# Kernel optimization log

Hardware: AMD Instinct MI355X
Metric: run time of the kernel (lower is better)

Reference implementation:

```python
import jax, jax.numpy as jnp
import numpy as np

# ---- config (mirrors init_kwargs) ----
D_MODEL = 1024
D_STATE = 128
EXPAND = 2
HEADDIM = 64
D_INNER = D_MODEL * EXPAND            # 2048
NHEADS = D_INNER // HEADDIM           # 32
ROPE_FRACTION = 0.5
ROTATE_DIM = (int(D_STATE * ROPE_FRACTION) // 2) * 2   # 64
NUM_ANGLES = ROTATE_DIM // 2          # 32
A_FLOOR = 1e-4
EPS = 1e-5
IN_PROJ_DIM = 2 * D_INNER + 2 * D_STATE + 3 * NHEADS + NUM_ANGLES  # 4480
BATCH, SEQLEN = 2, 2048


def _state_rmsnorm(x, w):
    rms = jnp.sqrt(jnp.mean(x * x, axis=-1, keepdims=True) + EPS)
    return x / rms * w


def _apply_rotary_pairs(x, phase):
    # x: (b,s,h,d_state), phase: (b,s,h,num_pairs)
    if ROTATE_DIM == 0:
        return x
    x_rot = x[..., :ROTATE_DIM].reshape(*x.shape[:-1], ROTATE_DIM // 2, 2)
    x_pass = x[..., ROTATE_DIM:]
    cos = jnp.cos(phase)
    sin = jnp.sin(phase)
    real = x_rot[..., 0]
    imag = x_rot[..., 1]
    rr = real * cos - imag * sin
    ri = real * sin + imag * cos
    rotated = jnp.stack([rr, ri], axis=-1).reshape(*x.shape[:-1], ROTATE_DIM)
    if x_pass.shape[-1] == 0:
        return rotated
    return jnp.concatenate([rotated, x_pass], axis=-1)


def setup_inputs() -> dict:
    key = jax.random.key(0)
    ks = jax.random.split(key, 5)
    x = jax.random.normal(ks[0], (BATCH, SEQLEN, D_MODEL), jnp.float32)
    W_in = jax.random.normal(ks[1], (IN_PROJ_DIM, D_MODEL), jnp.float32) / np.sqrt(D_MODEL)
    # dt_bias ~ inverse-softplus of dt sampled in [dt_min, dt_max]
    dt = jnp.exp(jax.random.uniform(ks[2], (NHEADS,), jnp.float32) * (np.log(0.1) - np.log(0.001)) + np.log(0.001))
    dt = jnp.clip(dt, 1e-4)
    dt_bias = dt + jnp.log(-jnp.expm1(-dt))
    B_norm_w = jnp.ones((D_STATE,), jnp.float32)
    C_norm_w = jnp.ones((D_STATE,), jnp.float32)
    B_bias = jnp.ones((NHEADS, D_STATE), jnp.float32)
    C_bias = jnp.ones((NHEADS, D_STATE), jnp.float32)
    D_param = jnp.ones((NHEADS,), jnp.float32)
    out_norm_w = jnp.ones((D_INNER,), jnp.float32)
    W_out = jax.random.normal(ks[3], (D_MODEL, D_INNER), jnp.float32) / np.sqrt(D_INNER)
    return {"x": x, "W_in": W_in, "dt_bias": dt_bias, "B_norm_w": B_norm_w,
            "C_norm_w": C_norm_w, "B_bias": B_bias, "C_bias": C_bias,
            "D_param": D_param, "out_norm_w": out_norm_w, "W_out": W_out}


def reference(x, W_in, dt_bias, B_norm_w, C_norm_w, B_bias, C_bias, D_param, out_norm_w, W_out):
    b, s, _ = x.shape
    proj = jnp.einsum('bsd,pd->bsp', x, W_in)
    sizes = [D_INNER, D_INNER, D_STATE, D_STATE, NHEADS, NHEADS, NHEADS, NUM_ANGLES]
    offs = np.cumsum([0] + sizes)
    z, v, B_raw, C_raw, dd_dt, dd_A, trap_logits, angle_logits = [
        proj[..., offs[i]:offs[i + 1]] for i in range(8)]
    z = z.reshape(b, s, NHEADS, HEADDIM)
    v = v.reshape(b, s, NHEADS, HEADDIM)
    Bm = _state_rmsnorm(B_raw, B_norm_w)[:, :, None, :] + B_bias[None, None]   # (b,s,h,n)
    Cm = _state_rmsnorm(C_raw, C_norm_w)[:, :, None, :] + C_bias[None, None]
    dt = jax.nn.softplus(dd_dt + dt_bias[None, None])          # (b,s,h)
    A = jnp.minimum(-jax.nn.softplus(dd_A), -A_FLOOR)          # (b,s,h)
    trap = jax.nn.sigmoid(trap_logits)                          # (b,s,h)
    phase = jnp.cumsum(angle_logits, axis=1)[:, :, None, :]     # (b,s,1,angles)
    phase = jnp.broadcast_to(phase, (b, s, NHEADS, NUM_ANGLES))
    Bm = _apply_rotary_pairs(Bm, phase)
    Cm = _apply_rotary_pairs(Cm, phase)

    alpha = jnp.exp(A * dt)               # (b,s,h)
    beta = (1.0 - trap) * dt * alpha
    gamma = trap * dt

    # move time to leading for scan: (s, b, h, ...)
    def tl(a):
        return jnp.moveaxis(a, 1, 0)
    xs = (tl(alpha), tl(beta), tl(gamma), tl(Bm), tl(Cm), tl(v))

    state0 = jnp.zeros((b, NHEADS, HEADDIM, D_STATE), jnp.float32)
    pk0 = jnp.zeros((b, NHEADS, D_STATE), jnp.float32)
    pv0 = jnp.zeros((b, NHEADS, HEADDIM), jnp.float32)

    def step(carry, inp):
        state, pk, pv = carry
        a_t, b_t, g_t, k_t, q_t, v_t = inp
        prev_outer = pv[..., :, None] * pk[..., None, :]        # (b,h,p,n)
        curr_outer = v_t[..., :, None] * k_t[..., None, :]
        state = (a_t[..., None, None] * state
                 + b_t[..., None, None] * prev_outer
                 + g_t[..., None, None] * curr_outer)
        y_t = jnp.einsum('bhpn,bhn->bhp', state, q_t) + D_param[None, :, None] * v_t
        return (state, k_t, v_t), y_t

    _, ys = jax.lax.scan(step, (state0, pk0, pv0), xs)
    y = jnp.moveaxis(ys, 0, 1).reshape(b, s, D_INNER)
    z = z.reshape(b, s, D_INNER)
    # GatedRMSNorm
    rms = jnp.sqrt(jnp.mean(y * y, axis=-1, keepdims=True) + EPS)
    y = (y / rms * out_norm_w) * jax.nn.silu(z)
    return jnp.einsum('bsi,di->bsd', y, W_out)
```

## Files before the change

### kernel.cpp

```cpp
#include <hip/hip_runtime.h>
#include <math.h>

#define S_LEN 2048
#define NBATCH 2
#define DMODEL 1024
#define PDIM 4480
#define DI 2048
#define NH 32
#define HD 64
#define DS 128
#define NA 32
#define CHK 64
#define NC (S_LEN / CHK)
#define OFF_Z 0
#define OFF_V 2048
#define OFF_B 4096
#define OFF_C 4224
#define OFF_DT 4352
#define OFF_A 4384
#define OFF_TRAP 4416
#define OFF_ANG 4448

typedef __attribute__((ext_vector_type(8))) short s8v;
typedef __attribute__((ext_vector_type(4))) float f4v;

__device__ __forceinline__ float softplus_f(float x) {
    return x > 20.f ? x : log1pf(expf(x));
}

__device__ __forceinline__ ushort f2bf(float f) {
    unsigned u = __float_as_uint(f);
    unsigned r = (u + 0x7fffu + ((u >> 16) & 1u)) >> 16;
    return (ushort)r;
}

__device__ __forceinline__ uint4 pack8(const float* f) {
    uint4 o;
    o.x = (unsigned)f2bf(f[0]) | ((unsigned)f2bf(f[1]) << 16);
    o.y = (unsigned)f2bf(f[2]) | ((unsigned)f2bf(f[3]) << 16);
    o.z = (unsigned)f2bf(f[4]) | ((unsigned)f2bf(f[5]) << 16);
    o.w = (unsigned)f2bf(f[6]) | ((unsigned)f2bf(f[7]) << 16);
    return o;
}

__device__ __forceinline__ float bf2f(ushort u) {
    unsigned v = ((unsigned)u) << 16;
    return __uint_as_float(v);
}

__global__ __launch_bounds__(256)
void f2bf_swz(const float* __restrict__ in, ushort* __restrict__ out,
              int nchunks, int shift) {
    int idx = blockIdx.x * 256 + threadIdx.x;
    if (idx >= nchunks) return;
    int dst = idx ^ ((idx >> shift) & 7);
    const float* ip = in + (size_t)idx * 8;
    float4 v0 = *(const float4*)ip;
    float4 v1 = *(const float4*)(ip + 4);
    uint4 o;
    o.x = (unsigned)f2bf(v0.x) | ((unsigned)f2bf(v0.y) << 16);
    o.y = (unsigned)f2bf(v0.z) | ((unsigned)f2bf(v0.w) << 16);
    o.z = (unsigned)f2bf(v1.x) | ((unsigned)f2bf(v1.y) << 16);
    o.w = (unsigned)f2bf(v1.z) | ((unsigned)f2bf(v1.w) << 16);
    *(uint4*)(out + (size_t)dst * 8) = o;
}

__global__ __launch_bounds__(256, 2)
void gemm_bf16(const ushort* __restrict__ A, const ushort* __restrict__ B,
               float* __restrict__ C, int M, int N, int K) {
    __shared__ __align__(16) short lA[128 * 64];
    __shared__ __align__(16) short lB[128 * 64];
    int nwg = gridDim.x;
    int bid = blockIdx.x;
    int q = nwg >> 3;
    int swz = (bid & 7) * q + (bid >> 3);
    int nb = N >> 7;
    int bx = swz % nb, by = swz / nb;

    int tid = threadIdx.x;
    int wv = tid >> 6, ln = tid & 63;
    int rl = ln & 15, kg = ln >> 4, r7 = rl & 7;
    int R0 = (wv >> 1) * 64, C0 = (wv & 1) * 64;

    const ushort* Ag = A + (size_t)(by * 128 + wv * 32 + (ln >> 3)) * K + (ln & 7) * 8;
    const ushort* Bg = B + (size_t)(bx * 128 + wv * 32 + (ln >> 3)) * K + (ln & 7) * 8;
    short* lAw = lA + (wv * 32) * 64;
    short* lBw = lB + (wv * 32) * 64;

    f4v acc[4][4];
#pragma unroll
    for (int m = 0; m < 4; ++m)
#pragma unroll
        for (int n = 0; n < 4; ++n) acc[m][n] = f4v{0.f, 0.f, 0.f, 0.f};

    for (int k0 = 0; k0 < K; k0 += 64) {
        __syncthreads();
#pragma unroll
        for (int i = 0; i < 4; ++i) {
            __builtin_amdgcn_global_load_lds(
                (const __attribute__((address_space(1))) void*)(Ag + (size_t)i * 8 * K + k0),
                (__attribute__((address_space(3))) void*)(lAw + i * 8 * 64), 16, 0, 0);
            __builtin_amdgcn_global_load_lds(
                (const __attribute__((address_space(1))) void*)(Bg + (size_t)i * 8 * K + k0),
                (__attribute__((address_space(3))) void*)(lBw + i * 8 * 64), 16, 0, 0);
        }
        __syncthreads();
#pragma unroll
        for (int ks = 0; ks < 2; ++ks) {
            int kc = ks * 4 + kg;
            int co = ((kc ^ r7) << 3);
            s8v av[4], bv[4];
#pragma unroll
            for (int m = 0; m < 4; ++m)
                av[m] = *(const s8v*)&lA[(R0 + m * 16 + rl) * 64 + co];
#pragma unroll
            for (int n = 0; n < 4; ++n)
                bv[n] = *(const s8v*)&lB[(C0 + n * 16 + rl) * 64 + co];
#pragma unroll
            for (int m = 0; m < 4; ++m)
#pragma unroll
                for (int n = 0; n < 4; ++n)
                    acc[m][n] = __builtin_amdgcn_mfma_f32_16x16x32_bf16(
                        av[m], bv[n], acc[m][n], 0, 0, 0);
        }
    }
#pragma unroll
    for (int m = 0; m < 4; ++m)
#pragma unroll
        for (int n = 0; n < 4; ++n) {
            size_t row0 = (size_t)(by * 128 + R0 + m * 16 + kg * 4);
            int col = bx * 128 + C0 + n * 16 + rl;
#pragma unroll
            for (int r = 0; r < 4; ++r)
                C[(row0 + r) * N + col] = acc[m][n][r];
        }
}

__global__ __launch_bounds__(256)
void phase_kernel(const float* __restrict__ proj, float* __restrict__ cosb,
                  float* __restrict__ sinb) {
    int b = blockIdx.x >> 5;
    int j = blockIdx.x & 31;
    int tid = threadIdx.x;
    __shared__ float part[256];
    float v[8];
    float run = 0.f;
#pragma unroll
    for (int e = 0; e < 8; ++e) {
        int s = tid * 8 + e;
        v[e] = proj[((size_t)(b * S_LEN + s)) * PDIM + OFF_ANG + j];
        run += v[e];
    }
    part[tid] = run;
    __syncthreads();
    for (int off = 1; off < 256; off <<= 1) {
        float add = (tid >= off) ? part[tid - off] : 0.f;
        __syncthreads();
        part[tid] += add;
        __syncthreads();
    }
    float acc = (tid > 0) ? part[tid - 1] : 0.f;
#pragma unroll
    for (int e = 0; e < 8; ++e) {
        acc += v[e];
        int s = tid * 8 + e;
        size_t o = ((size_t)(b * S_LEN + s)) * NA + j;
        cosb[o] = cosf(acc);
        sinb[o] = sinf(acc);
    }
}

__global__ __launch_bounds__(128)
void prep_kernel(const float* __restrict__ proj, const float* __restrict__ dt_bias,
                 const float* __restrict__ Bw, const float* __restrict__ Cw,
                 const float* __restrict__ cosb, const float* __restrict__ sinb,
                 float* __restrict__ Bn, float* __restrict__ Cn,
                 float* __restrict__ ldb, float* __restrict__ wbuf,
                 float* __restrict__ pubuf) {
    size_t row = blockIdx.x;
    int b = (int)(row >> 11);
    int s = (int)(row & 2047);
    int n = threadIdx.x;
    const float* pr = proj + row * PDIM;
    float vB = pr[OFF_B + n];
    float vC = pr[OFF_C + n];
    float sB = vB * vB, sC = vC * vC;
#pragma unroll
    for (int off = 32; off >= 1; off >>= 1) {
        sB += __shfl_xor(sB, off);
        sC += __shfl_xor(sC, off);
    }
    __shared__ float redB[2], redC[2];
    if ((n & 63) == 0) { redB[n >> 6] = sB; redC[n >> 6] = sC; }
    __syncthreads();
    float rB = sqrtf((redB[0] + redB[1]) * (1.f / 128.f) + 1e-5f);
    float rC = sqrtf((redC[0] + redC[1]) * (1.f / 128.f) + 1e-5f);
    float bn = vB / rB * Bw[n];
    float cn = vC / rC * Cw[n];
    float bp = __shfl_xor(bn, 1);
    float cp = __shfl_xor(cn, 1);
    float ob = bn, oc = cn;
    if (n < 64) {
        float c = cosb[row * NA + (n >> 1)];
        float sn_ = sinb[row * NA + (n >> 1)];
        if ((n & 1) == 0) { ob = bn * c - bp * sn_; oc = cn * c - cp * sn_; }
        else              { ob = bp * sn_ + bn * c; oc = cp * sn_ + cn * c; }
    }
    Bn[row * DS + n] = ob;
    Cn[row * DS + n] = oc;
    if (n < NH) {
        int h = n;
        float dtv = softplus_f(pr[OFF_DT + h] + dt_bias[h]);
        float Av = -fmaxf(softplus_f(pr[OFF_A + h]), 1e-4f);
        float trap = 1.f / (1.f + expf(-pr[OFF_TRAP + h]));
        size_t o = ((size_t)(b * NH + h)) * S_LEN + s;
        ldb[o]   = Av * dtv;
        wbuf[o]  = trap * dtv;
        pubuf[o] = (1.f - trap) * dtv;
    }
}

__global__ __launch_bounds__(256)
void lcum_kernel(float* __restrict__ ell) {
    size_t row = blockIdx.x;
    int tid = threadIdx.x;
    float* p = ell + row * S_LEN;
    float v[8];
    float run = 0.f;
#pragma unroll
    for (int e = 0; e < 8; ++e) { v[e] = p[tid * 8 + e]; run += v[e]; }
    __shared__ float part[256];
    part[tid] = run;
    __syncthreads();
    for (int off = 1; off < 256; off <<= 1) {
        float add = (tid >= off) ? part[tid - off] : 0.f;
        __syncthreads();
        part[tid] += add;
        __syncthreads();
    }
    float acc = (tid > 0) ? part[tid - 1] : 0.f;
#pragma unroll
    for (int e = 0; e < 8; ++e) { acc += v[e]; p[tid * 8 + e] = acc; }
}

__device__ __forceinline__ void build_vals32(
    float* vals, const float* __restrict__ br, const float* __restrict__ bias,
    const float* __restrict__ cr, const float* __restrict__ sr, int n0, int rot) {
    if (rot) {
#pragma unroll
        for (int a = 0; a < 16; ++a) {
            float c = cr[a], s = sr[a];
            float e = bias[n0 + 2 * a], o = bias[n0 + 2 * a + 1];
            vals[2 * a]     = br[2 * a]     + e * c - o * s;
            vals[2 * a + 1] = br[2 * a + 1] + e * s + o * c;
        }
    } else {
#pragma unroll
        for (int j = 0; j < 32; ++j) vals[j] = br[j] + bias[n0 + j];
    }
}

__global__ __launch_bounds__(256, 2)
void delta_kernel(const float* __restrict__ proj, const float* __restrict__ Bn,
                  const float* __restrict__ cosb, const float* __restrict__ sinb,
                  const float* __restrict__ ell, const float* __restrict__ wbuf,
                  const float* __restrict__ pubuf, const float* __restrict__ B_bias,
                  float* __restrict__ delta, float* __restrict__ rbuf) {
    __shared__ ushort KT[DS * CHK];
    __shared__ ushort VT[HD * CHK];
    int blk = blockIdx.x;
    int c = blk & (NC - 1);
    int h = (blk >> 5) & (NH - 1);
    int b = blk >> 10;
    int tid = threadIdx.x;
    size_t row0 = (size_t)b * S_LEN + c * CHK;
    size_t bh = (size_t)b * NH + h;
    int i = tid >> 2, q4 = tid & 3;

    size_t so = bh * S_LEN + c * CHK + i;
    float llast = ell[bh * S_LEN + c * CHK + CHK - 1];
    float u = wbuf[so];
    if (c * CHK + i < S_LEN - 1) u += pubuf[so + 1];
    float coef = expf(llast - ell[so]) * u;
    if (tid == 0) {
        float base = (c == 0) ? 0.f : ell[bh * S_LEN + c * CHK - 1];
        rbuf[blk] = expf(llast - base);
    }
    {
        int n0 = q4 * 32;
        float vals[32];
        build_vals32(vals, Bn + (row0 + i) * DS + n0, B_bias + h * DS,
                     cosb + (row0 + i) * NA + q4 * 16, sinb + (row0 + i) * NA + q4 * 16,
                     n0, q4 < 2);
#pragma unroll
        for (int j = 0; j < 32; ++j) {
            int n = n0 + j;
            KT[n * 64 + (((i >> 3) ^ (n & 7)) << 3) + (i & 7)] = f2bf(vals[j]);
        }
    }
    {
        int p0 = q4 * 16;
        const float* vr = proj + (row0 + i) * PDIM + OFF_V + h * HD + p0;
#pragma unroll
        for (int j = 0; j < 16; ++j) {
            int p = p0 + j;
            VT[p * 64 + (((i >> 3) ^ (p & 7)) << 3) + (i & 7)] = f2bf(vr[j] * coef);
        }
    }
    __syncthreads();
    int wv = tid >> 6, ln = tid & 63, rl = ln & 15, kg = ln >> 4;
    int pA = wv * 16 + rl;
    s8v aV[2];
#pragma unroll
    for (int ks = 0; ks < 2; ++ks)
        aV[ks] = *(const s8v*)&VT[pA * 64 + (((ks * 4 + kg) ^ (pA & 7)) << 3)];
    f4v dacc[8];
#pragma unroll
    for (int nt = 0; nt < 8; ++nt) dacc[nt] = f4v{0.f, 0.f, 0.f, 0.f};
#pragma unroll
    for (int nt = 0; nt < 8; ++nt) {
        int nB = nt * 16 + rl;
#pragma unroll
        for (int ks = 0; ks < 2; ++ks) {
            s8v bK = *(const s8v*)&KT[nB * 64 + (((ks * 4 + kg) ^ (nB & 7)) << 3)];
            dacc[nt] = __builtin_amdgcn_mfma_f32_16x16x32_bf16(aV[ks], bK, dacc[nt], 0, 0, 0);
        }
    }
    float* dp = delta + (bh * NC + c) * (size_t)(HD * DS);
#pragma unroll
    for (int nt = 0; nt < 8; ++nt) {
        int n = nt * 16 + rl;
#pragma unroll
        for (int r = 0; r < 4; ++r) {
            int p = wv * 16 + kg * 4 + r;
            dp[p * DS + n] = dacc[nt][r];
        }
    }
}

__global__ __launch_bounds__(256)
void state_prop(float* __restrict__ delta, const float* __restrict__ rbuf) {
    size_t bh = blockIdx.x;
    int tid = threadIdx.x;
    float4 st[8];
#pragma unroll
    for (int k = 0; k < 8; ++k) st[k] = float4{0.f, 0.f, 0.f, 0.f};
    for (int c = 0; c < NC; ++c) {
        float* dp = delta + (bh * NC + c) * (size_t)(HD * DS);
        float r = rbuf[bh * NC + c];
#pragma unroll
        for (int k = 0; k < 8; ++k) {
            int off = k * 1024 + tid * 4;
            float4 d = *(const float4*)(dp + off);
            float4 s = st[k];
            *(float4*)(dp + off) = s;
            st[k].x = fmaf(r, s.x, d.x);
            st[k].y = fmaf(r, s.y, d.y);
            st[k].z = fmaf(r, s.z, d.z);
            st[k].w = fmaf(r, s.w, d.w);
        }
    }
}

__global__ __launch_bounds__(256, 2)
void out_kernel(const float* __restrict__ proj, const float* __restrict__ Bn,
                const float* __restrict__ Cn, const float* __restrict__ cosb,
                const float* __restrict__ sinb, const float* __restrict__ ell,
                const float* __restrict__ wbuf, const float* __restrict__ pubuf,
                const float* __restrict__ B_bias, const float* __restrict__ C_bias,
                const float* __restrict__ D_param, const float* __restrict__ delta,
                float* __restrict__ y) {
    __shared__ ushort Qb[CHK * DS];
    __shared__ ushort Kb[CHK * DS];
    __shared__ ushort VTb[HD * CHK];
    __shared__ ushort PTb[CHK * CHK];
    __shared__ float s_ell[CHK], s_u[CHK], s_w[CHK], s_d[CHK];
    int blk = blockIdx.x;
    int c = blk & (NC - 1);
    int h = (blk >> 5) & (NH - 1);
    int b = blk >> 10;
    int tid = threadIdx.x;
    size_t row0 = (size_t)b * S_LEN + c * CHK;
    size_t bh = (size_t)b * NH + h;

    const float* sp0 = delta + (bh * NC + c) * (size_t)(HD * DS)
                       + (size_t)(tid >> 2) * DS + (tid & 3) * 32;
    float4 sreg[8];
#pragma unroll
    for (int j = 0; j < 8; ++j) sreg[j] = ((const float4*)sp0)[j];

    int t = tid >> 2, q4 = tid & 3;
    {
        int n0 = q4 * 32;
        float vals[32];
        build_vals32(vals, Cn + (row0 + t) * DS + n0, C_bias + h * DS,
                     cosb + (row0 + t) * NA + q4 * 16, sinb + (row0 + t) * NA + q4 * 16,
                     n0, q4 < 2);
#pragma unroll
        for (int j = 0; j < 4; ++j) {
            int cc = (q4 * 4 + j) ^ (t & 7);
            *(uint4*)&Qb[t * 128 + cc * 8] = pack8(&vals[j * 8]);
        }
    }
    {
        int n0 = q4 * 32;
        float vals[32];
        build_vals32(vals, Bn + (row0 + t) * DS + n0, B_bias + h * DS,
                     cosb + (row0 + t) * NA + q4 * 16, sinb + (row0 + t) * NA + q4 * 16,
                     n0, q4 < 2);
#pragma unroll
        for (int j = 0; j < 4; ++j) {
            int cc = (q4 * 4 + j) ^ (t & 7);
            *(uint4*)&Kb[t * 128 + cc * 8] = pack8(&vals[j * 8]);
        }
    }
    {
        int p0 = q4 * 16;
        const float* vr = proj + (row0 + t) * PDIM + OFF_V + h * HD + p0;
#pragma unroll
        for (int j = 0; j < 16; ++j) {
            int p = p0 + j;
            VTb[p * 64 + (((t >> 3) ^ (p & 7)) << 3) + (t & 7)] = f2bf(vr[j]);
        }
    }
    if (tid < CHK) {
        int tt = tid;
        size_t so = bh * S_LEN + c * CHK + tt;
        float lt = ell[so];
        s_ell[tt] = lt;
        float wv_ = wbuf[so];
        s_w[tt] = wv_;
        float u = wv_;
        if (c * CHK + tt < S_LEN - 1) u += pubuf[so + 1];
        s_u[tt] = u;
        float base = (c == 0) ? 0.f : ell[bh * S_LEN + c * CHK - 1];
        s_d[tt] = expf(lt - base);
    }
    __syncthreads();

    int wv = tid >> 6, ln = tid & 63, rl = ln & 15, kg = ln >> 4;
    int tA = wv * 16 + rl;
    s8v aQ[4];
#pragma unroll
    for (int kc = 0; kc < 4; ++kc)
        aQ[kc] = *(const s8v*)&Qb[tA * 128 + (((kc * 4 + kg) ^ (tA & 7)) << 3)];
    f4v pacc[4];
#pragma unroll
    for (int st = 0; st < 4; ++st) pacc[st] = f4v{0.f, 0.f, 0.f, 0.f};
#pragma unroll
    for (int st = 0; st < 4; ++st) {
        int sB = st * 16 + rl;
#pragma unroll
        for (int kc = 0; kc < 4; ++kc) {
            s8v bK = *(const s8v*)&Kb[sB * 128 + (((kc * 4 + kg) ^ (sB & 7)) << 3)];
            pacc[st] = __builtin_amdgcn_mfma_f32_16x16x32_bf16(aQ[kc], bK, pacc[st], 0, 0, 0);
        }
    }
#pragma unroll
    for (int st = 0; st < 4; ++st) {
        int s = st * 16 + rl;
#pragma unroll
        for (int r = 0; r < 4; ++r) {
            int t2 = wv * 16 + kg * 4 + r;
            float m;
            if (s < t2)       m = expf(s_ell[t2] - s_ell[s]) * s_u[s];
            else if (s == t2) m = s_w[t2];
            else              m = 0.f;
            PTb[t2 * 64 + (((s >> 3) ^ (t2 & 7)) << 3) + (s & 7)] = f2bf(pacc[st][r] * m);
        }
    }
    __syncthreads();
    {
        int p = tid >> 2, nq = tid & 3;
        float fv[32];
#pragma unroll
        for (int j = 0; j < 8; ++j) *(float4*)&fv[j * 4] = sreg[j];
#pragma unroll
        for (int j = 0; j < 4; ++j) {
            int cc = (nq * 4 + j) ^ (p & 7);
            *(uint4*)&Kb[p * 128 + cc * 8] = pack8(&fv[j * 8]);
        }
    }
    __syncthreads();
    s8v aP[2];
#pragma unroll
    for (int ks = 0; ks < 2; ++ks)
        aP[ks] = *(const s8v*)&PTb[tA * 64 + (((ks * 4 + kg) ^ (tA & 7)) << 3)];
    f4v y1[4], y2[4];
#pragma unroll
    for (int pt = 0; pt < 4; ++pt) { y1[pt] = f4v{0.f,0.f,0.f,0.f}; y2[pt] = f4v{0.f,0.f,0.f,0.f}; }
#pragma unroll
    for (int pt = 0; pt < 4; ++pt) {
        int pB = pt * 16 + rl;
#pragma unroll
        for (int ks = 0; ks < 2; ++ks) {
            s8v bV = *(const s8v*)&VTb[pB * 64 + (((ks * 4 + kg) ^ (pB & 7)) << 3)];
            y1[pt] = __builtin_amdgcn_mfma_f32_16x16x32_bf16(aP[ks], bV, y1[pt], 0, 0, 0);
        }
#pragma unroll
        for (int kc = 0; kc < 4; ++kc) {
            s8v bS = *(const s8v*)&Kb[pB * 128 + (((kc * 4 + kg) ^ (pB & 7)) << 3)];
            y2[pt] = __builtin_amdgcn_mfma_f32_16x16x32_bf16(aQ[kc], bS, y2[pt], 0, 0, 0);
        }
    }
    float Dp = D_param[h];
#pragma unroll
    for (int pt = 0; pt < 4; ++pt) {
#pragma unroll
        for (int r = 0; r < 4; ++r) {
            int t2 = wv * 16 + kg * 4 + r;
            int p = pt * 16 + rl;
            float v = proj[(row0 + t2) * PDIM + OFF_V + h * HD + p];
            y[(row0 + t2) * DI + h * HD + p] = y1[pt][r] + s_d[t2] * y2[pt][r] + Dp * v;
        }
    }
}

__global__ __launch_bounds__(256)
void ynorm_kernel(const float* __restrict__ y, const float* __restrict__ proj,
                  const float* __restrict__ w, ushort* __restrict__ ybf) {
    size_t row = blockIdx.x;
    int tid = threadIdx.x;
    const float* yr = y + row * (size_t)DI;
    float4 v0 = *(const float4*)(yr + tid * 8);
    float4 v1 = *(const float4*)(yr + tid * 8 + 4);
    float ss = v0.x * v0.x + v0.y * v0.y + v0.z * v0.z + v0.w * v0.w +
               v1.x * v1.x + v1.y * v1.y + v1.z * v1.z + v1.w * v1.w;
#pragma unroll
    for (int off = 32; off >= 1; off >>= 1) ss += __shfl_xor(ss, off);
    __shared__ float red[4];
    if ((tid & 63) == 0) red[tid >> 6] = ss;
    __syncthreads();
    float tot = red[0] + red[1] + red[2] + red[3];
    float rinv = 1.f / sqrtf(tot * (1.f / 2048.f) + 1e-5f);
    const float* zr = proj + row * (size_t)PDIM + OFF_Z;
    float4 z0 = *(const float4*)(zr + tid * 8);
    float4 z1 = *(const float4*)(zr + tid * 8 + 4);
    float4 w0 = *(const float4*)(w + tid * 8);
    float4 w1 = *(const float4*)(w + tid * 8 + 4);
    float yv[8] = {v0.x, v0.y, v0.z, v0.w, v1.x, v1.y, v1.z, v1.w};
    float zv[8] = {z0.x, z0.y, z0.z, z0.w, z1.x, z1.y, z1.z, z1.w};
    float wv[8] = {w0.x, w0.y, w0.z, w0.w, w1.x, w1.y, w1.z, w1.w};
    ushort u[8];
#pragma unroll
    for (int e = 0; e < 8; ++e) {
        float sil = zv[e] / (1.f + expf(-zv[e]));
        u[e] = f2bf(yv[e] * rinv * wv[e] * sil);
    }
    int dstc = (tid & ~7) | ((tid & 7) ^ ((int)row & 7));
    uint4 o;
    o.x = (unsigned)u[0] | ((unsigned)u[1] << 16);
    o.y = (unsigned)u[2] | ((unsigned)u[3] << 16);
    o.z = (unsigned)u[4] | ((unsigned)u[5] << 16);
    o.w = (unsigned)u[6] | ((unsigned)u[7] << 16);
    *(uint4*)(ybf + row * (size_t)DI + dstc * 8) = o;
}

extern "C" void kernel_launch(void* const* d_in, const int* in_sizes, int n_in,
                              void* d_out, int out_size, void* d_ws, size_t ws_size,
                              hipStream_t stream) {
    const float* x          = (const float*)d_in[0];
    const float* W_in       = (const float*)d_in[1];
    const float* dt_bias    = (const float*)d_in[2];
    const float* B_norm_w   = (const float*)d_in[3];
    const float* C_norm_w   = (const float*)d_in[4];
    const float* B_bias     = (const float*)d_in[5];
    const float* C_bias     = (const float*)d_in[6];
    const float* D_param    = (const float*)d_in[7];
    const float* out_norm_w = (const float*)d_in[8];
    const float* W_out      = (const float*)d_in[9];
    float* out = (float*)d_out;

    const size_t M = (size_t)NBATCH * S_LEN;
    float* ws = (float*)d_ws;
    size_t off = 0;
    float* proj  = ws + off; off += M * PDIM;
    float* cosb  = ws + off; off += M * NA;
    float* sinb  = ws + off; off += M * NA;
    float* Bn    = ws + off; off += M * DS;
    float* Cn    = ws + off; off += M * DS;
    float* ell   = ws + off; off += (size_t)NBATCH * NH * S_LEN;
    float* wbuf  = ws + off; off += (size_t)NBATCH * NH * S_LEN;
    float* pubuf = ws + off; off += (size_t)NBATCH * NH * S_LEN;
    float* delta = ws + off; off += (size_t)NBATCH * NH * NC * HD * DS;
    float* rbuf  = ws + off; off += (size_t)NBATCH * NH * NC;
    float* y     = ws + off; off += M * DI;
    ushort* xbf  = (ushort*)(ws + off); off += M * DMODEL / 2;
    ushort* wibf = (ushort*)(ws + off); off += (size_t)PDIM * DMODEL / 2;
    ushort* wobf = (ushort*)(ws + off); off += (size_t)DMODEL * DI / 2;
    ushort* ybf  = (ushort*)(ws + off); off += M * DI / 2;

    {
        int nc_x  = (int)(M * DMODEL / 8);
        int nc_wi = PDIM * DMODEL / 8;
        int nc_wo = DMODEL * DI / 8;
        f2bf_swz<<<dim3((nc_x + 255) / 256), 256, 0, stream>>>(x, xbf, nc_x, 7);
        f2bf_swz<<<dim3((nc_wi + 255) / 256), 256, 0, stream>>>(W_in, wibf, nc_wi, 7);
        f2bf_swz<<<dim3((nc_wo + 255) / 256), 256, 0, stream>>>(W_out, wobf, nc_wo, 8);
    }
    gemm_bf16<<<dim3((PDIM / 128) * (int)(M / 128)), 256, 0, stream>>>(xbf, wibf, proj, (int)M, PDIM, DMODEL);
    phase_kernel<<<dim3(NBATCH * NA), 256, 0, stream>>>(proj, cosb, sinb);
    prep_kernel<<<dim3((int)M), 128, 0, stream>>>(proj, dt_bias, B_norm_w, C_norm_w,
                                                  cosb, sinb, Bn, Cn, ell, wbuf, pubuf);
    lcum_kernel<<<dim3(NBATCH * NH), 256, 0, stream>>>(ell);
    delta_kernel<<<dim3(NBATCH * NH * NC), 256, 0, stream>>>(proj, Bn, cosb, sinb, ell,
                                                             wbuf, pubuf, B_bias, delta, rbuf);
    state_prop<<<dim3(NBATCH * NH), 256, 0, stream>>>(delta, rbuf);
    out_kernel<<<dim3(NBATCH * NH * NC), 256, 0, stream>>>(proj, Bn, Cn, cosb, sinb, ell,
                                                           wbuf, pubuf, B_bias, C_bias,
                                                           D_param, delta, y);
    ynorm_kernel<<<dim3((int)M), 256, 0, stream>>>(y, proj, out_norm_w, ybf);
    gemm_bf16<<<dim3((DMODEL / 128) * (int)(M / 128)), 256, 0, stream>>>(ybf, wobf, out, (int)M, DMODEL, DI);
}
```

Baseline: 267.0 us.

## Move intra-chunk work into the delta kernel and pass bf16 tiles to a lean output kernel

The delta kernel becomes bdp_kernel. It now builds Q, K and V once per chunk, computes the masked QK^T decay matrix and the chunk state delta, and writes bf16 Q, V, P and state tiles to workspace. State propagation now reads and writes bf16 states with register prefetch of the next chunk, which halves that traffic. The output kernel becomes out2_kernel, which loads the precomputed tiles straight into LDS with global_load_lds and only does the final two matmuls. This removes duplicated B/C rotation and V loading between the two chunk kernels, in exchange for extra bf16 round trips through global memory and lower state precision.

```diff
diff --git a/kernel.cpp b/kernel.cpp
--- a/kernel.cpp
+++ b/kernel.cpp
@@ -44,9 +44,10 @@
 }
 
 __device__ __forceinline__ float bf2f(ushort u) {
-    unsigned v = ((unsigned)u) << 16;
-    return __uint_as_float(v);
-}
+    return __uint_as_float(((unsigned)u) << 16);
+}
+__device__ __forceinline__ float bf_lo(unsigned u) { return __uint_as_float(u << 16); }
+__device__ __forceinline__ float bf_hi(unsigned u) { return __uint_as_float(u & 0xffff0000u); }
 
 __global__ __launch_bounds__(256)
 void f2bf_swz(const float* __restrict__ in, ushort* __restrict__ out,
@@ -260,14 +261,20 @@
     }
 }
 
-__global__ __launch_bounds__(256, 2)
-void delta_kernel(const float* __restrict__ proj, const float* __restrict__ Bn,
-                  const float* __restrict__ cosb, const float* __restrict__ sinb,
-                  const float* __restrict__ ell, const float* __restrict__ wbuf,
-                  const float* __restrict__ pubuf, const float* __restrict__ B_bias,
-                  float* __restrict__ delta, float* __restrict__ rbuf) {
-    __shared__ ushort KT[DS * CHK];
-    __shared__ ushort VT[HD * CHK];
+__global__ __launch_bounds__(256, 3)
+void bdp_kernel(const float* __restrict__ proj, const float* __restrict__ Bn,
+                const float* __restrict__ Cn, const float* __restrict__ cosb,
+                const float* __restrict__ sinb, const float* __restrict__ ell,
+                const float* __restrict__ wbuf, const float* __restrict__ pubuf,
+                const float* __restrict__ B_bias, const float* __restrict__ C_bias,
+                ushort* __restrict__ qbuf, ushort* __restrict__ vtbuf,
+                ushort* __restrict__ pbuf, ushort* __restrict__ dstate,
+                float* __restrict__ dvec, float* __restrict__ rbuf) {
+    __shared__ __align__(16) ushort Qb[CHK * DS];
+    __shared__ __align__(16) ushort Kb[CHK * DS];
+    __shared__ __align__(16) ushort cVT[HD * CHK];
+    __shared__ __align__(16) ushort PB[CHK * CHK];
+    __shared__ float s_ell[CHK], s_u[CHK], s_w[CHK];
     int blk = blockIdx.x;
     int c = blk & (NC - 1);
     int h = (blk >> 5) & (NH - 1);
@@ -279,13 +286,17 @@
 
     size_t so = bh * S_LEN + c * CHK + i;
     float llast = ell[bh * S_LEN + c * CHK + CHK - 1];
+    float li = ell[so];
     float u = wbuf[so];
     if (c * CHK + i < S_LEN - 1) u += pubuf[so + 1];
-    float coef = expf(llast - ell[so]) * u;
-    if (tid == 0) {
-        float base = (c == 0) ? 0.f : ell[bh * S_LEN + c * CHK - 1];
-        rbuf[blk] = expf(llast - base);
-    }
+    float coef = expf(llast - li) * u;
+    float base = (c == 0) ? 0.f : ell[bh * S_LEN + c * CHK - 1];
+    if (q4 == 0) {
+        s_ell[i] = li; s_u[i] = u; s_w[i] = wbuf[so];
+        dvec[(size_t)blk * CHK + i] = expf(li - base);
+    }
+    if (tid == 0) rbuf[blk] = expf(llast - base);
+
     {
         int n0 = q4 * 32;
         float vals[32];
@@ -293,9 +304,21 @@
                      cosb + (row0 + i) * NA + q4 * 16, sinb + (row0 + i) * NA + q4 * 16,
                      n0, q4 < 2);
 #pragma unroll
-        for (int j = 0; j < 32; ++j) {
-            int n = n0 + j;
-            KT[n * 64 + (((i >> 3) ^ (n & 7)) << 3) + (i & 7)] = f2bf(vals[j]);
+        for (int j = 0; j < 4; ++j) {
+            int cc = (q4 * 4 + j) ^ (i & 7);
+            *(uint4*)&Kb[i * 128 + cc * 8] = pack8(&vals[j * 8]);
+        }
+    }
+    {
+        int n0 = q4 * 32;
+        float vals[32];
+        build_vals32(vals, Cn + (row0 + i) * DS + n0, C_bias + h * DS,
+                     cosb + (row0 + i) * NA + q4 * 16, sinb + (row0 + i) * NA + q4 * 16,
+                     n0, q4 < 2);
+#pragma unroll
+        for (int j = 0; j < 4; ++j) {
+            int cc = (q4 * 4 + j) ^ (i & 7);
+            *(uint4*)&Qb[i * 128 + cc * 8] = pack8(&vals[j * 8]);
         }
     }
     {
@@ -304,156 +327,54 @@
 #pragma unroll
         for (int j = 0; j < 16; ++j) {
             int p = p0 + j;
-            VT[p * 64 + (((i >> 3) ^ (p & 7)) << 3) + (i & 7)] = f2bf(vr[j] * coef);
-        }
-    }
-    __syncthreads();
+            float v = vr[j];
+            int addr = p * 64 + (((i >> 3) ^ (p & 7)) << 3) + (i & 7);
+            PB[addr]  = f2bf(v);
+            cVT[addr] = f2bf(v * coef);
+        }
+    }
+    __syncthreads();
+
     int wv = tid >> 6, ln = tid & 63, rl = ln & 15, kg = ln >> 4;
-    int pA = wv * 16 + rl;
-    s8v aV[2];
-#pragma unroll
-    for (int ks = 0; ks < 2; ++ks)
-        aV[ks] = *(const s8v*)&VT[pA * 64 + (((ks * 4 + kg) ^ (pA & 7)) << 3)];
-    f4v dacc[8];
-#pragma unroll
-    for (int nt = 0; nt < 8; ++nt) dacc[nt] = f4v{0.f, 0.f, 0.f, 0.f};
-#pragma unroll
-    for (int nt = 0; nt < 8; ++nt) {
-        int nB = nt * 16 + rl;
-#pragma unroll
-        for (int ks = 0; ks < 2; ++ks) {
-            s8v bK = *(const s8v*)&KT[nB * 64 + (((ks * 4 + kg) ^ (nB & 7)) << 3)];
-            dacc[nt] = __builtin_amdgcn_mfma_f32_16x16x32_bf16(aV[ks], bK, dacc[nt], 0, 0, 0);
-        }
-    }
-    float* dp = delta + (bh * NC + c) * (size_t)(HD * DS);
-#pragma unroll
-    for (int nt = 0; nt < 8; ++nt) {
-        int n = nt * 16 + rl;
-#pragma unroll
-        for (int r = 0; r < 4; ++r) {
-            int p = wv * 16 + kg * 4 + r;
-            dp[p * DS + n] = dacc[nt][r];
-        }
-    }
-}
-
-__global__ __launch_bounds__(256)
-void state_prop(float* __restrict__ delta, const float* __restrict__ rbuf) {
-    size_t bh = blockIdx.x;
-    int tid = threadIdx.x;
-    float4 st[8];
-#pragma unroll
-    for (int k = 0; k < 8; ++k) st[k] = float4{0.f, 0.f, 0.f, 0.f};
-    for (int c = 0; c < NC; ++c) {
-        float* dp = delta + (bh * NC + c) * (size_t)(HD * DS);
-        float r = rbuf[bh * NC + c];
-#pragma unroll
-        for (int k = 0; k < 8; ++k) {
-            int off = k * 1024 + tid * 4;
-            float4 d = *(const float4*)(dp + off);
-            float4 s = st[k];
-            *(float4*)(dp + off) = s;
-            st[k].x = fmaf(r, s.x, d.x);
-            st[k].y = fmaf(r, s.y, d.y);
-            st[k].z = fmaf(r, s.z, d.z);
-            st[k].w = fmaf(r, s.w, d.w);
-        }
-    }
-}
-
-__global__ __launch_bounds__(256, 2)
-void out_kernel(const float* __restrict__ proj, const float* __restrict__ Bn,
-                const float* __restrict__ Cn, const float* __restrict__ cosb,
-                const float* __restrict__ sinb, const float* __restrict__ ell,
-                const float* __restrict__ wbuf, const float* __restrict__ pubuf,
-                const float* __restrict__ B_bias, const float* __restrict__ C_bias,
-                const float* __restrict__ D_param, const float* __restrict__ delta,
-                float* __restrict__ y) {
-    __shared__ ushort Qb[CHK * DS];
-    __shared__ ushort Kb[CHK * DS];
-    __shared__ ushort VTb[HD * CHK];
-    __shared__ ushort PTb[CHK * CHK];
-    __shared__ float s_ell[CHK], s_u[CHK], s_w[CHK], s_d[CHK];
-    int blk = blockIdx.x;
-    int c = blk & (NC - 1);
-    int h = (blk >> 5) & (NH - 1);
-    int b = blk >> 10;
-    int tid = threadIdx.x;
-    size_t row0 = (size_t)b * S_LEN + c * CHK;
-    size_t bh = (size_t)b * NH + h;
-
-    const float* sp0 = delta + (bh * NC + c) * (size_t)(HD * DS)
-                       + (size_t)(tid >> 2) * DS + (tid & 3) * 32;
-    float4 sreg[8];
-#pragma unroll
-    for (int j = 0; j < 8; ++j) sreg[j] = ((const float4*)sp0)[j];
-
-    int t = tid >> 2, q4 = tid & 3;
+    int tA = wv * 16 + rl;
+    s8v aQ[4];
+#pragma unroll
+    for (int kc = 0; kc < 4; ++kc)
+        aQ[kc] = *(const s8v*)&Qb[tA * 128 + (((kc * 4 + kg) ^ (tA & 7)) << 3)];
+    f4v pacc[4];
+#pragma unroll
+    for (int st = 0; st < 4; ++st) pacc[st] = f4v{0.f, 0.f, 0.f, 0.f};
+#pragma unroll
+    for (int st = 0; st < 4; ++st) {
+        int sB = st * 16 + rl;
+#pragma unroll
+        for (int kc = 0; kc < 4; ++kc) {
+            s8v bK = *(const s8v*)&Kb[sB * 128 + (((kc * 4 + kg) ^ (sB & 7)) << 3)];
+            pacc[st] = __builtin_amdgcn_mfma_f32_16x16x32_bf16(aQ[kc], bK, pacc[st], 0, 0, 0);
+        }
+    }
+    {
+        const uint4* qs = (const uint4*)Qb;
+        uint4* qd = (uint4*)(qbuf + (size_t)blk * (CHK * DS));
+#pragma unroll
+        for (int k = 0; k < 4; ++k) qd[tid + k * 256] = qs[tid + k * 256];
+        const uint4* vs = (const uint4*)PB;
+        uint4* vd = (uint4*)(vtbuf + (size_t)blk * (CHK * CHK));
+#pragma unroll
+        for (int k = 0; k < 2; ++k) vd[tid + k * 256] = vs[tid + k * 256];
+    }
+    __syncthreads();
+
     {
         int n0 = q4 * 32;
         float vals[32];
-        build_vals32(vals, Cn + (row0 + t) * DS + n0, C_bias + h * DS,
-                     cosb + (row0 + t) * NA + q4 * 16, sinb + (row0 + t) * NA + q4 * 16,
+        build_vals32(vals, Bn + (row0 + i) * DS + n0, B_bias + h * DS,
+                     cosb + (row0 + i) * NA + q4 * 16, sinb + (row0 + i) * NA + q4 * 16,
                      n0, q4 < 2);
 #pragma unroll
-        for (int j = 0; j < 4; ++j) {
-            int cc = (q4 * 4 + j) ^ (t & 7);
-            *(uint4*)&Qb[t * 128 + cc * 8] = pack8(&vals[j * 8]);
-        }
-    }
-    {
-        int n0 = q4 * 32;
-        float vals[32];
-        build_vals32(vals, Bn + (row0 + t) * DS + n0, B_bias + h * DS,
-                     cosb + (row0 + t) * NA + q4 * 16, sinb + (row0 + t) * NA + q4 * 16,
-                     n0, q4 < 2);
-#pragma unroll
-        for (int j = 0; j < 4; ++j) {
-            int cc = (q4 * 4 + j) ^ (t & 7);
-            *(uint4*)&Kb[t * 128 + cc * 8] = pack8(&vals[j * 8]);
-        }
-    }
-    {
-        int p0 = q4 * 16;
-        const float* vr = proj + (row0 + t) * PDIM + OFF_V + h * HD + p0;
-#pragma unroll
-        for (int j = 0; j < 16; ++j) {
-            int p = p0 + j;
-            VTb[p * 64 + (((t >> 3) ^ (p & 7)) << 3) + (t & 7)] = f2bf(vr[j]);
-        }
-    }
-    if (tid < CHK) {
-        int tt = tid;
-        size_t so = bh * S_LEN + c * CHK + tt;
-        float lt = ell[so];
-        s_ell[tt] = lt;
-        float wv_ = wbuf[so];
-        s_w[tt] = wv_;
-        float u = wv_;
-        if (c * CHK + tt < S_LEN - 1) u += pubuf[so + 1];
-        s_u[tt] = u;
-        float base = (c == 0) ? 0.f : ell[bh * S_LEN + c * CHK - 1];
-        s_d[tt] = expf(lt - base);
-    }
-    __syncthreads();
-
-    int wv = tid >> 6, ln = tid & 63, rl = ln & 15, kg = ln >> 4;
-    int tA = wv * 16 + rl;
-    s8v aQ[4];
-#pragma unroll
-    for (int kc = 0; kc < 4; ++kc)
-        aQ[kc] = *(const s8v*)&Qb[tA * 128 + (((kc * 4 + kg) ^ (tA & 7)) << 3)];
-    f4v pacc[4];
-#pragma unroll
-    for (int st = 0; st < 4; ++st) pacc[st] = f4v{0.f, 0.f, 0.f, 0.f};
-#pragma unroll
-    for (int st = 0; st < 4; ++st) {
-        int sB = st * 16 + rl;
-#pragma unroll
-        for (int kc = 0; kc < 4; ++kc) {
-            s8v bK = *(const s8v*)&Kb[sB * 128 + (((kc * 4 + kg) ^ (sB & 7)) << 3)];
-            pacc[st] = __builtin_amdgcn_mfma_f32_16x16x32_bf16(aQ[kc], bK, pacc[st], 0, 0, 0);
+        for (int j = 0; j < 32; ++j) {
+            int n = n0 + j;
+            Qb[n * 64 + (((i >> 3) ^ (n & 7)) << 3) + (i & 7)] = f2bf(vals[j]);
         }
     }
 #pragma unroll
@@ -466,22 +387,140 @@
             if (s < t2)       m = expf(s_ell[t2] - s_ell[s]) * s_u[s];
             else if (s == t2) m = s_w[t2];
             else              m = 0.f;
-            PTb[t2 * 64 + (((s >> 3) ^ (t2 & 7)) << 3) + (s & 7)] = f2bf(pacc[st][r] * m);
-        }
-    }
-    __syncthreads();
+            PB[t2 * 64 + (((s >> 3) ^ (t2 & 7)) << 3) + (s & 7)] = f2bf(pacc[st][r] * m);
+        }
+    }
+    __syncthreads();
+
+    int pA = wv * 16 + rl;
+    s8v aV[2];
+#pragma unroll
+    for (int ks = 0; ks < 2; ++ks)
+        aV[ks] = *(const s8v*)&cVT[pA * 64 + (((ks * 4 + kg) ^ (pA & 7)) << 3)];
+#pragma unroll
+    for (int nt = 0; nt < 8; ++nt) {
+        int nB = nt * 16 + rl;
+        f4v dacc = f4v{0.f, 0.f, 0.f, 0.f};
+#pragma unroll
+        for (int ks = 0; ks < 2; ++ks) {
+            s8v bK = *(const s8v*)&Qb[nB * 64 + (((ks * 4 + kg) ^ (nB & 7)) << 3)];
+            dacc = __builtin_amdgcn_mfma_f32_16x16x32_bf16(aV[ks], bK, dacc, 0, 0, 0);
+        }
+#pragma unroll
+        for (int r = 0; r < 4; ++r) {
+            int p = wv * 16 + kg * 4 + r;
+            int n = nt * 16 + rl;
+            Kb[p * 128 + (((n >> 3) ^ (p & 7)) << 3) + (n & 7)] = f2bf(dacc[r]);
+        }
+    }
+    __syncthreads();
+
     {
-        int p = tid >> 2, nq = tid & 3;
-        float fv[32];
-#pragma unroll
-        for (int j = 0; j < 8; ++j) *(float4*)&fv[j * 4] = sreg[j];
+        const uint4* ds_ = (const uint4*)Kb;
+        uint4* dd = (uint4*)(dstate + (size_t)blk * (CHK * DS));
+#pragma unroll
+        for (int k = 0; k < 4; ++k) dd[tid + k * 256] = ds_[tid + k * 256];
+        const uint4* ps = (const uint4*)PB;
+        uint4* pd = (uint4*)(pbuf + (size_t)blk * (CHK * CHK));
+#pragma unroll
+        for (int k = 0; k < 2; ++k) pd[tid + k * 256] = ps[tid + k * 256];
+    }
+}
+
+__global__ __launch_bounds__(256)
+void state_prop(ushort* __restrict__ dstate, const float* __restrict__ rbuf) {
+    size_t bh = blockIdx.x;
+    int tid = threadIdx.x;
+    float st[32];
+#pragma unroll
+    for (int j = 0; j < 32; ++j) st[j] = 0.f;
+    uint4* base = (uint4*)dstate;
+    size_t b0 = bh * NC * 1024ull;
+    uint4 nxt[4];
+#pragma unroll
+    for (int j = 0; j < 4; ++j) nxt[j] = base[b0 + tid * 4 + j];
+    for (int c = 0; c < NC; ++c) {
+        uint4 cur[4];
+#pragma unroll
+        for (int j = 0; j < 4; ++j) cur[j] = nxt[j];
+        if (c + 1 < NC) {
+#pragma unroll
+            for (int j = 0; j < 4; ++j)
+                nxt[j] = base[b0 + (size_t)(c + 1) * 1024 + tid * 4 + j];
+        }
+        float r = rbuf[bh * NC + c];
+        uint4 outv[4];
 #pragma unroll
         for (int j = 0; j < 4; ++j) {
-            int cc = (nq * 4 + j) ^ (p & 7);
-            *(uint4*)&Kb[p * 128 + cc * 8] = pack8(&fv[j * 8]);
-        }
-    }
-    __syncthreads();
+            unsigned uu[4] = {cur[j].x, cur[j].y, cur[j].z, cur[j].w};
+            unsigned oo[4];
+#pragma unroll
+            for (int e = 0; e < 4; ++e) {
+                float d0 = bf_lo(uu[e]), d1 = bf_hi(uu[e]);
+                int ix = j * 8 + e * 2;
+                oo[e] = (unsigned)f2bf(st[ix]) | ((unsigned)f2bf(st[ix + 1]) << 16);
+                st[ix]     = fmaf(r, st[ix], d0);
+                st[ix + 1] = fmaf(r, st[ix + 1], d1);
+            }
+            outv[j] = uint4{oo[0], oo[1], oo[2], oo[3]};
+        }
+#pragma unroll
+        for (int j = 0; j < 4; ++j)
+            base[b0 + (size_t)c * 1024 + tid * 4 + j] = outv[j];
+    }
+}
+
+__global__ __launch_bounds__(256, 3)
+void out2_kernel(const ushort* __restrict__ qbuf, const ushort* __restrict__ vtbuf,
+                 const ushort* __restrict__ pbuf, const ushort* __restrict__ dstate,
+                 const float* __restrict__ dvec, const float* __restrict__ D_param,
+                 float* __restrict__ y) {
+    __shared__ __align__(16) ushort Qb[CHK * DS];
+    __shared__ __align__(16) ushort Sb[CHK * DS];
+    __shared__ __align__(16) ushort PTb[CHK * CHK];
+    __shared__ __align__(16) ushort VTb[CHK * CHK];
+    __shared__ float s_d[CHK];
+    int blk = blockIdx.x;
+    int c = blk & (NC - 1);
+    int h = (blk >> 5) & (NH - 1);
+    int b = blk >> 10;
+    int tid = threadIdx.x;
+    int wv = tid >> 6, ln = tid & 63;
+    size_t row0 = (size_t)b * S_LEN + c * CHK;
+
+    const ushort* qg = qbuf + (size_t)blk * (CHK * DS);
+    const ushort* sg = dstate + (size_t)blk * (CHK * DS);
+    const ushort* pg = pbuf + (size_t)blk * (CHK * CHK);
+    const ushort* vg = vtbuf + (size_t)blk * (CHK * CHK);
+#pragma unroll
+    for (int k = 0; k < 4; ++k) {
+        int ch = wv * 256 + k * 64;
+        __builtin_amdgcn_global_load_lds(
+            (const __attribute__((address_space(1))) void*)(qg + (size_t)(ch + ln) * 8),
+            (__attribute__((address_space(3))) void*)(Qb + ch * 8), 16, 0, 0);
+        __builtin_amdgcn_global_load_lds(
+            (const __attribute__((address_space(1))) void*)(sg + (size_t)(ch + ln) * 8),
+            (__attribute__((address_space(3))) void*)(Sb + ch * 8), 16, 0, 0);
+    }
+#pragma unroll
+    for (int k = 0; k < 2; ++k) {
+        int ch = wv * 128 + k * 64;
+        __builtin_amdgcn_global_load_lds(
+            (const __attribute__((address_space(1))) void*)(pg + (size_t)(ch + ln) * 8),
+            (__attribute__((address_space(3))) void*)(PTb + ch * 8), 16, 0, 0);
+        __builtin_amdgcn_global_load_lds(
+            (const __attribute__((address_space(1))) void*)(vg + (size_t)(ch + ln) * 8),
+            (__attribute__((address_space(3))) void*)(VTb + ch * 8), 16, 0, 0);
+    }
+    if (tid < CHK) s_d[tid] = dvec[(size_t)blk * CHK + tid];
+    __syncthreads();
+
+    int rl = ln & 15, kg = ln >> 4;
+    int tA = wv * 16 + rl;
+    s8v aQ[4];
+#pragma unroll
+    for (int kc = 0; kc < 4; ++kc)
+        aQ[kc] = *(const s8v*)&Qb[tA * 128 + (((kc * 4 + kg) ^ (tA & 7)) << 3)];
     s8v aP[2];
 #pragma unroll
     for (int ks = 0; ks < 2; ++ks)
@@ -499,7 +538,7 @@
         }
 #pragma unroll
         for (int kc = 0; kc < 4; ++kc) {
-            s8v bS = *(const s8v*)&Kb[pB * 128 + (((kc * 4 + kg) ^ (pB & 7)) << 3)];
+            s8v bS = *(const s8v*)&Sb[pB * 128 + (((kc * 4 + kg) ^ (pB & 7)) << 3)];
             y2[pt] = __builtin_amdgcn_mfma_f32_16x16x32_bf16(aQ[kc], bS, y2[pt], 0, 0, 0);
         }
     }
@@ -510,7 +549,7 @@
         for (int r = 0; r < 4; ++r) {
             int t2 = wv * 16 + kg * 4 + r;
             int p = pt * 16 + rl;
-            float v = proj[(row0 + t2) * PDIM + OFF_V + h * HD + p];
+            float v = bf2f(VTb[p * 64 + (((t2 >> 3) ^ (p & 7)) << 3) + (t2 & 7)]);
             y[(row0 + t2) * DI + h * HD + p] = y1[pt][r] + s_d[t2] * y2[pt][r] + Dp * v;
         }
     }
@@ -572,6 +611,7 @@
     float* out = (float*)d_out;
 
     const size_t M = (size_t)NBATCH * S_LEN;
+    const size_t NBLK = (size_t)NBATCH * NH * NC;
     float* ws = (float*)d_ws;
     size_t off = 0;
     float* proj  = ws + off; off += M * PDIM;
@@ -582,13 +622,17 @@
     float* ell   = ws + off; off += (size_t)NBATCH * NH * S_LEN;
     float* wbuf  = ws + off; off += (size_t)NBATCH * NH * S_LEN;
     float* pubuf = ws + off; off += (size_t)NBATCH * NH * S_LEN;
-    float* delta = ws + off; off += (size_t)NBATCH * NH * NC * HD * DS;
-    float* rbuf  = ws + off; off += (size_t)NBATCH * NH * NC;
     float* y     = ws + off; off += M * DI;
+    float* rbuf  = ws + off; off += NBLK;
+    float* dvec  = ws + off; off += NBLK * CHK;
     ushort* xbf  = (ushort*)(ws + off); off += M * DMODEL / 2;
     ushort* wibf = (ushort*)(ws + off); off += (size_t)PDIM * DMODEL / 2;
     ushort* wobf = (ushort*)(ws + off); off += (size_t)DMODEL * DI / 2;
     ushort* ybf  = (ushort*)(ws + off); off += M * DI / 2;
+    ushort* qbuf   = (ushort*)(ws + off); off += NBLK * CHK * DS / 2;
+    ushort* dstate = (ushort*)(ws + off); off += NBLK * CHK * DS / 2;
+    ushort* pbuf   = (ushort*)(ws + off); off += NBLK * CHK * CHK / 2;
+    ushort* vtbuf  = (ushort*)(ws + off); off += NBLK * CHK * CHK / 2;
 
     {
         int nc_x  = (int)(M * DMODEL / 8);
@@ -603,12 +647,12 @@
     prep_kernel<<<dim3((int)M), 128, 0, stream>>>(proj, dt_bias, B_norm_w, C_norm_w,
                                                   cosb, sinb, Bn, Cn, ell, wbuf, pubuf);
     lcum_kernel<<<dim3(NBATCH * NH), 256, 0, stream>>>(ell);
-    delta_kernel<<<dim3(NBATCH * NH * NC), 256, 0, stream>>>(proj, Bn, cosb, sinb, ell,
-                                                             wbuf, pubuf, B_bias, delta, rbuf);
-    state_prop<<<dim3(NBATCH * NH), 256, 0, stream>>>(delta, rbuf);
-    out_kernel<<<dim3(NBATCH * NH * NC), 256, 0, stream>>>(proj, Bn, Cn, cosb, sinb, ell,
-                                                           wbuf, pubuf, B_bias, C_bias,
-                                                           D_param, delta, y);
+    bdp_kernel<<<dim3((int)NBLK), 256, 0, stream>>>(proj, Bn, Cn, cosb, sinb, ell,
+                                                    wbuf, pubuf, B_bias, C_bias,
+                                                    qbuf, vtbuf, pbuf, dstate, dvec, rbuf);
+    state_prop<<<dim3(NBATCH * NH), 256, 0, stream>>>(dstate, rbuf);
+    out2_kernel<<<dim3((int)NBLK), 256, 0, stream>>>(qbuf, vtbuf, pbuf, dstate,
+                                                     dvec, D_param, y);
     ynorm_kernel<<<dim3((int)M), 256, 0, stream>>>(y, proj, out_norm_w, ybf);
     gemm_bf16<<<dim3((DMODEL / 128) * (int)(M / 128)), 256, 0, stream>>>(ybf, wobf, out, (int)M, DMODEL, DI);
 }
```

New measurement: 273.5 us. 1.02x slower.
